# Optimization experiments

Hardware: AMD Instinct MI355X
Metric: run time of the kernel (lower is better)

## Reference

```python
import jax, jax.numpy as jnp
import numpy as np

NUM_HEADS = 8
NUM_POINTS = 4


def setup_inputs() -> dict:
    key = jax.random.key(0)
    bs, h, w = 2, 128, 128
    cin = cout = 256
    nq = h * w
    ks = jax.random.split(key, 6)
    query = jax.random.normal(ks[0], (bs, nq, cin), jnp.float32)
    value = jax.random.normal(ks[1], (bs, nq, cin), jnp.float32)
    # sampling_offsets: small random weight, bias = directional grid init (as in init_weights)
    W_off = jax.random.normal(ks[2], (cin, NUM_HEADS * NUM_POINTS * 2), jnp.float32) * 0.01
    thetas = np.arange(NUM_HEADS, dtype=np.float32) * (2.0 * np.pi / NUM_HEADS)
    grid = np.stack([np.cos(thetas), np.sin(thetas)], -1)
    grid = grid / np.abs(grid).max(-1, keepdims=True)
    grid = np.tile(grid[:, None, :], (1, NUM_POINTS, 1)) * (np.arange(NUM_POINTS, dtype=np.float32)[None, :, None] + 1.0)
    b_off = jnp.asarray(grid.reshape(-1), jnp.float32)
    W_attn = jax.random.normal(ks[3], (cin, NUM_HEADS * NUM_POINTS), jnp.float32) * 0.01
    b_attn = jnp.zeros((NUM_HEADS * NUM_POINTS,), jnp.float32)
    s = 1.0 / np.sqrt(cin)  # xavier-ish uniform
    W_val = jax.random.uniform(ks[4], (cin, cout), jnp.float32, -s, s)
    b_val = jnp.zeros((cout,), jnp.float32)
    W_out = jax.random.uniform(ks[5], (cout, cout), jnp.float32, -s, s)
    b_out = jnp.zeros((cout,), jnp.float32)
    return {"query": query, "value": value, "W_off": W_off, "b_off": b_off,
            "W_attn": W_attn, "b_attn": b_attn, "W_val": W_val, "b_val": b_val,
            "W_out": W_out, "b_out": b_out, "h": h, "w": w}


def _bilinear_sample(v_flat, ix, iy, h, w):
    # v_flat: (bs, heads, h*w, d); ix/iy: (bs, heads, nq, P) pixel coords.
    # grid_sample bilinear, align_corners=False, padding_mode='zeros'.
    x0 = jnp.floor(ix)
    y0 = jnp.floor(iy)
    wx1 = ix - x0
    wy1 = iy - y0
    bs, hd, nq, P = ix.shape
    acc = 0.0
    corners = ((x0, y0, (1.0 - wx1) * (1.0 - wy1)),
               (x0 + 1.0, y0, wx1 * (1.0 - wy1)),
               (x0, y0 + 1.0, (1.0 - wx1) * wy1),
               (x0 + 1.0, y0 + 1.0, wx1 * wy1))
    for xc, yc, wgt in corners:
        xi = xc.astype(jnp.int32)
        yi = yc.astype(jnp.int32)
        valid = (xi >= 0) & (xi < w) & (yi >= 0) & (yi < h)
        idx = jnp.clip(yi, 0, h - 1) * w + jnp.clip(xi, 0, w - 1)
        g = jnp.take_along_axis(v_flat, idx.reshape(bs, hd, nq * P)[..., None], axis=2)
        acc = acc + g.reshape(bs, hd, nq, P, -1) * (wgt * valid)[..., None]
    return acc  # (bs, heads, nq, P, d)


def deform_attn(query, value, W_off, b_off, W_attn, b_attn, W_val, b_val, h, w):
    bs, nq, _ = query.shape
    d = W_val.shape[1] // NUM_HEADS
    v = (value @ W_val + b_val).reshape(bs, nq, NUM_HEADS, d)
    off = (query @ W_off + b_off).reshape(bs, nq, NUM_HEADS, NUM_POINTS, 2)
    aw = jax.nn.softmax((query @ W_attn + b_attn).reshape(bs, nq, NUM_HEADS, NUM_POINTS), axis=-1)
    # reference points in [0,1], scale_ratio=1.0, (x, y) order
    ys = (jnp.arange(h, dtype=jnp.float32) + 0.5) / h
    xs = (jnp.arange(w, dtype=jnp.float32) + 0.5) / w
    ry, rx = jnp.meshgrid(ys, xs, indexing='ij')
    ref = jnp.stack([rx.reshape(-1), ry.reshape(-1)], -1)  # (nq, 2)
    loc = ref[None, :, None, None, :] + off / jnp.array([w, h], jnp.float32)
    grid = 2.0 * loc - 1.0  # normalized grid_sample coords
    grid = grid.transpose(0, 2, 1, 3, 4)  # (bs, heads, nq, P, 2)
    ix = (grid[..., 0] + 1.0) * (w / 2.0) - 0.5
    iy = (grid[..., 1] + 1.0) * (h / 2.0) - 0.5
    v_flat = v.transpose(0, 2, 1, 3)  # (bs, heads, h*w, d)
    sampled = _bilinear_sample(v_flat, ix, iy, h, w)  # (bs, heads, nq, P, d)
    out = (sampled * aw.transpose(0, 2, 1, 3)[..., None]).sum(3)  # (bs, heads, nq, d)
    return out.transpose(0, 2, 1, 3).reshape(bs, nq, NUM_HEADS * d)


def reference(query, value, W_off, b_off, W_attn, b_attn, W_val, b_val, W_out, b_out, h, w):
    attn = deform_attn(query, value, W_off, b_off, W_attn, b_attn, W_val, b_val, h, w)
    # dropout acts as identity in eval mode; identity residual = query
    return attn @ W_out + b_out + query
```

## Files before the change

kernel.cpp:

```cpp
#include <hip/hip_runtime.h>
#include <type_traits>

#define H_IMG 128
#define W_IMG 128
#define NQ (H_IMG * W_IMG)
#define CIN 256
#define NH 8
#define NP 4
#define DH 32
#define LDSP 264

typedef __bf16 bf16x4 __attribute__((ext_vector_type(4)));
typedef __bf16 bf16x8 __attribute__((ext_vector_type(8)));
typedef float f32x4 __attribute__((ext_vector_type(4)));

__global__ __launch_bounds__(256) void prep_weights(
    const float* __restrict__ Wval, const float* __restrict__ Wout,
    const float* __restrict__ Woff, const float* __restrict__ Wattn,
    const float* __restrict__ boff, const float* __restrict__ battn,
    __bf16* __restrict__ btv, __bf16* __restrict__ bto,
    __bf16* __restrict__ btoa, float* __restrict__ bias96) {
  int id = blockIdx.x * 256 + threadIdx.x;
  if (id < 256 * 256) {
    int n = id >> 8, k = id & 255;
    btv[n * 256 + k] = (__bf16)Wval[k * 256 + n];
    bto[n * 256 + k] = (__bf16)Wout[k * 256 + n];
  }
  if (id < 96 * 256) {
    int n = id >> 8, k = id & 255;
    float w = (n < 64) ? Woff[k * 64 + n] : Wattn[k * 32 + (n - 64)];
    btoa[n * 256 + k] = (__bf16)w;
  }
  if (id < 96) {
    bias96[id] = (id < 64) ? boff[id] : battn[id - 64];
  }
}

template <typename TA, typename TC, bool PLANAR, bool ADD>
__global__ __launch_bounds__(256) void gemm64(
    const TA* __restrict__ A, const __bf16* __restrict__ BT,
    const float* __restrict__ bias, const float* __restrict__ addm,
    TC* __restrict__ C, int M) {
  const int t = threadIdx.x;
  const int lane = t & 63;
  const int wave = t >> 6;
  const int r = lane & 15;
  const int q = lane >> 4;
  const int gm0 = blockIdx.x * 64;
  const int gn0 = blockIdx.y * 64;
  const int wm = (wave & 1) * 32;
  const int wn = (wave >> 1) * 32;

  __shared__ __bf16 As[64 * LDSP];
  __shared__ __bf16 Bs[64 * LDSP];

  if constexpr (std::is_same<TA, float>::value) {
#pragma unroll
    for (int i = 0; i < 16; ++i) {
      int g = i * 256 + t;
      int row = g >> 6, c4 = g & 63;
      float4 f = *(const float4*)(A + (size_t)(gm0 + row) * 256 + c4 * 4);
      bf16x4 hh;
      hh[0] = (__bf16)f.x; hh[1] = (__bf16)f.y;
      hh[2] = (__bf16)f.z; hh[3] = (__bf16)f.w;
      *(bf16x4*)(&As[row * LDSP + c4 * 4]) = hh;
    }
  } else {
#pragma unroll
    for (int i = 0; i < 8; ++i) {
      int g = i * 256 + t;
      int row = g >> 5, c = g & 31;
      *(bf16x8*)(&As[row * LDSP + c * 8]) =
          *(const bf16x8*)(A + (size_t)(gm0 + row) * 256 + c * 8);
    }
  }
#pragma unroll
  for (int i = 0; i < 8; ++i) {
    int g = i * 256 + t;
    int row = g >> 5, c = g & 31;
    *(bf16x8*)(&Bs[row * LDSP + c * 8]) =
        *(const bf16x8*)(BT + (size_t)(gn0 + row) * 256 + c * 8);
  }
  __syncthreads();

  f32x4 acc[2][2];
#pragma unroll
  for (int mt = 0; mt < 2; ++mt)
#pragma unroll
    for (int nt = 0; nt < 2; ++nt) acc[mt][nt] = (f32x4){0.f, 0.f, 0.f, 0.f};

#pragma unroll
  for (int kt = 0; kt < 8; ++kt) {
    const int ko = kt * 32 + q * 8;
    bf16x8 a0 = *(const bf16x8*)(&As[(wm + r) * LDSP + ko]);
    bf16x8 a1 = *(const bf16x8*)(&As[(wm + 16 + r) * LDSP + ko]);
    bf16x8 b0 = *(const bf16x8*)(&Bs[(wn + r) * LDSP + ko]);
    bf16x8 b1 = *(const bf16x8*)(&Bs[(wn + 16 + r) * LDSP + ko]);
    acc[0][0] = __builtin_amdgcn_mfma_f32_16x16x32_bf16(a0, b0, acc[0][0], 0, 0, 0);
    acc[0][1] = __builtin_amdgcn_mfma_f32_16x16x32_bf16(a0, b1, acc[0][1], 0, 0, 0);
    acc[1][0] = __builtin_amdgcn_mfma_f32_16x16x32_bf16(a1, b0, acc[1][0], 0, 0, 0);
    acc[1][1] = __builtin_amdgcn_mfma_f32_16x16x32_bf16(a1, b1, acc[1][1], 0, 0, 0);
  }

#pragma unroll
  for (int mt = 0; mt < 2; ++mt)
#pragma unroll
    for (int nt = 0; nt < 2; ++nt)
#pragma unroll
      for (int rr = 0; rr < 4; ++rr) {
        int row = gm0 + wm + mt * 16 + q * 4 + rr;
        int col = gn0 + wn + nt * 16 + r;
        float val = acc[mt][nt][rr] + bias[col];
        if constexpr (ADD) val += addm[(size_t)row * 256 + col];
        if constexpr (PLANAR)
          C[((size_t)(col >> 5) * M + row) * 32 + (col & 31)] = (TC)val;
        else
          C[(size_t)row * 256 + col] = (TC)val;
      }
}

__global__ __launch_bounds__(256) void oa_sample(
    const float* __restrict__ query, const __bf16* __restrict__ btoa,
    const float* __restrict__ bias96, const __bf16* __restrict__ v,
    __bf16* __restrict__ attn, int M) {
  const int t = threadIdx.x;
  const int lane = t & 63;
  const int wave = t >> 6;
  const int r = lane & 15;
  const int q = lane >> 4;
  const int gm0 = blockIdx.x * 64;
  const int wm = (wave & 1) * 32;
  const int n0 = (wave >> 1) * 48;

  __shared__ __bf16 As[64 * LDSP];
  __shared__ float oas[64 * 100];

#pragma unroll
  for (int i = 0; i < 16; ++i) {
    int g = i * 256 + t;
    int row = g >> 6, c4 = g & 63;
    float4 f = *(const float4*)(query + (size_t)(gm0 + row) * 256 + c4 * 4);
    bf16x4 hh;
    hh[0] = (__bf16)f.x; hh[1] = (__bf16)f.y;
    hh[2] = (__bf16)f.z; hh[3] = (__bf16)f.w;
    *(bf16x4*)(&As[row * LDSP + c4 * 4]) = hh;
  }
  __syncthreads();

  f32x4 acc[2][3];
#pragma unroll
  for (int mt = 0; mt < 2; ++mt)
#pragma unroll
    for (int nt = 0; nt < 3; ++nt) acc[mt][nt] = (f32x4){0.f, 0.f, 0.f, 0.f};

#pragma unroll
  for (int kt = 0; kt < 8; ++kt) {
    const int ko = kt * 32 + q * 8;
    bf16x8 a0 = *(const bf16x8*)(&As[(wm + r) * LDSP + ko]);
    bf16x8 a1 = *(const bf16x8*)(&As[(wm + 16 + r) * LDSP + ko]);
    bf16x8 b[3];
#pragma unroll
    for (int nt = 0; nt < 3; ++nt)
      b[nt] = *(const bf16x8*)(btoa + (size_t)(n0 + nt * 16 + r) * 256 + ko);
#pragma unroll
    for (int nt = 0; nt < 3; ++nt) {
      acc[0][nt] = __builtin_amdgcn_mfma_f32_16x16x32_bf16(a0, b[nt], acc[0][nt], 0, 0, 0);
      acc[1][nt] = __builtin_amdgcn_mfma_f32_16x16x32_bf16(a1, b[nt], acc[1][nt], 0, 0, 0);
    }
  }
#pragma unroll
  for (int mt = 0; mt < 2; ++mt)
#pragma unroll
    for (int nt = 0; nt < 3; ++nt)
#pragma unroll
      for (int rr = 0; rr < 4; ++rr) {
        int rl = wm + mt * 16 + q * 4 + rr;
        int col = n0 + nt * 16 + r;
        oas[rl * 100 + col] = acc[mt][nt][rr] + bias96[col];
      }
  __syncthreads();

  const int qrow = t >> 2;
  const int c8 = (t & 3) * 8;
  const int row = gm0 + qrow;
  const int b = row >> 14;
  const int qi = row & (NQ - 1);
  const int x = qi & (W_IMG - 1);
  const int y = qi >> 7;
  const float* oar = &oas[qrow * 100];
#pragma unroll
  for (int h = 0; h < NH; ++h) {
    float l0 = oar[64 + h * 4 + 0];
    float l1 = oar[64 + h * 4 + 1];
    float l2 = oar[64 + h * 4 + 2];
    float l3 = oar[64 + h * 4 + 3];
    float mx = fmaxf(fmaxf(l0, l1), fmaxf(l2, l3));
    float e0 = __expf(l0 - mx), e1 = __expf(l1 - mx);
    float e2 = __expf(l2 - mx), e3 = __expf(l3 - mx);
    float inv = 1.f / (e0 + e1 + e2 + e3);
    float awp[4] = {e0 * inv, e1 * inv, e2 * inv, e3 * inv};
    float fa[8] = {0.f, 0.f, 0.f, 0.f, 0.f, 0.f, 0.f, 0.f};
    const __bf16* vh = v + ((size_t)h * M + (size_t)b * NQ) * 32 + c8;
#pragma unroll
    for (int p = 0; p < NP; ++p) {
      float ox = oar[h * 8 + p * 2 + 0];
      float oy = oar[h * 8 + p * 2 + 1];
      float ix = (float)x + ox;
      float iy = (float)y + oy;
      float x0f = floorf(ix), y0f = floorf(iy);
      float wx1 = ix - x0f, wy1 = iy - y0f;
      int x0 = (int)x0f, y0 = (int)y0f;
      float wgt[4] = {(1.f - wx1) * (1.f - wy1), wx1 * (1.f - wy1),
                      (1.f - wx1) * wy1, wx1 * wy1};
      int xs[4] = {x0, x0 + 1, x0, x0 + 1};
      int ysv[4] = {y0, y0, y0 + 1, y0 + 1};
#pragma unroll
      for (int c = 0; c < 4; ++c) {
        int xi = xs[c], yi = ysv[c];
        bool valid = (xi >= 0) & (xi < W_IMG) & (yi >= 0) & (yi < H_IMG);
        int xc = xi < 0 ? 0 : (xi > W_IMG - 1 ? W_IMG - 1 : xi);
        int yc = yi < 0 ? 0 : (yi > H_IMG - 1 ? H_IMG - 1 : yi);
        float wv = awp[p] * wgt[c] * (valid ? 1.f : 0.f);
        bf16x8 g = *(const bf16x8*)(vh + (size_t)(yc * W_IMG + xc) * 32);
#pragma unroll
        for (int j = 0; j < 8; ++j) fa[j] += wv * (float)g[j];
      }
    }
    bf16x8 o;
#pragma unroll
    for (int j = 0; j < 8; ++j) o[j] = (__bf16)fa[j];
    *(bf16x8*)(attn + (size_t)row * 256 + h * DH + c8) = o;
  }
}

extern "C" void kernel_launch(void* const* d_in, const int* in_sizes, int n_in,
                              void* d_out, int out_size, void* d_ws, size_t ws_size,
                              hipStream_t stream) {
  const float* query  = (const float*)d_in[0];
  const float* value  = (const float*)d_in[1];
  const float* W_off  = (const float*)d_in[2];
  const float* b_off  = (const float*)d_in[3];
  const float* W_attn = (const float*)d_in[4];
  const float* b_attn = (const float*)d_in[5];
  const float* W_val  = (const float*)d_in[6];
  const float* b_val  = (const float*)d_in[7];
  const float* W_out  = (const float*)d_in[8];
  const float* b_out  = (const float*)d_in[9];
  float* out = (float*)d_out;

  char* ws = (char*)d_ws;
  __bf16* btv    = (__bf16*)(ws + 0);
  __bf16* bto    = (__bf16*)(ws + 131072);
  __bf16* btoa   = (__bf16*)(ws + 262144);
  float*  bias96 = (float*)(ws + 311296);
  __bf16* v      = (__bf16*)(ws + 524288);
  __bf16* attn   = (__bf16*)(ws + 17301504);

  const int M = in_sizes[0] / CIN;

  prep_weights<<<256, 256, 0, stream>>>(W_val, W_out, W_off, W_attn,
                                        b_off, b_attn, btv, bto, btoa, bias96);
  gemm64<float, __bf16, true, false><<<dim3(M / 64, 4), 256, 0, stream>>>(
      value, btv, b_val, nullptr, v, M);
  oa_sample<<<M / 64, 256, 0, stream>>>(query, btoa, bias96, v, attn, M);
  gemm64<__bf16, float, false, true><<<dim3(M / 64, 4), 256, 0, stream>>>(
      attn, bto, b_out, query, out, M);
}
```

Before: 175.0 us.

## Fuse output projection into sampling kernel and widen value GEMM tiles

```diff
diff --git a/kernel.cpp b/kernel.cpp
--- a/kernel.cpp
+++ b/kernel.cpp
@@ -1,5 +1,4 @@
 #include <hip/hip_runtime.h>
-#include <type_traits>
 
 #define H_IMG 128
 #define W_IMG 128
@@ -36,101 +35,79 @@
   }
 }
 
-template <typename TA, typename TC, bool PLANAR, bool ADD>
-__global__ __launch_bounds__(256) void gemm64(
-    const TA* __restrict__ A, const __bf16* __restrict__ BT,
-    const float* __restrict__ bias, const float* __restrict__ addm,
-    TC* __restrict__ C, int M) {
+__global__ __launch_bounds__(256) void gemm_v(
+    const float* __restrict__ A, const __bf16* __restrict__ BT,
+    const float* __restrict__ bias, __bf16* __restrict__ v, int M) {
   const int t = threadIdx.x;
   const int lane = t & 63;
   const int wave = t >> 6;
   const int r = lane & 15;
   const int q = lane >> 4;
   const int gm0 = blockIdx.x * 64;
-  const int gn0 = blockIdx.y * 64;
-  const int wm = (wave & 1) * 32;
-  const int wn = (wave >> 1) * 32;
+  const int wn = wave * 64;
 
   __shared__ __bf16 As[64 * LDSP];
-  __shared__ __bf16 Bs[64 * LDSP];
-
-  if constexpr (std::is_same<TA, float>::value) {
-#pragma unroll
-    for (int i = 0; i < 16; ++i) {
-      int g = i * 256 + t;
-      int row = g >> 6, c4 = g & 63;
-      float4 f = *(const float4*)(A + (size_t)(gm0 + row) * 256 + c4 * 4);
-      bf16x4 hh;
-      hh[0] = (__bf16)f.x; hh[1] = (__bf16)f.y;
-      hh[2] = (__bf16)f.z; hh[3] = (__bf16)f.w;
-      *(bf16x4*)(&As[row * LDSP + c4 * 4]) = hh;
-    }
-  } else {
-#pragma unroll
-    for (int i = 0; i < 8; ++i) {
-      int g = i * 256 + t;
-      int row = g >> 5, c = g & 31;
-      *(bf16x8*)(&As[row * LDSP + c * 8]) =
-          *(const bf16x8*)(A + (size_t)(gm0 + row) * 256 + c * 8);
-    }
-  }
-#pragma unroll
-  for (int i = 0; i < 8; ++i) {
+
+#pragma unroll
+  for (int i = 0; i < 16; ++i) {
     int g = i * 256 + t;
-    int row = g >> 5, c = g & 31;
-    *(bf16x8*)(&Bs[row * LDSP + c * 8]) =
-        *(const bf16x8*)(BT + (size_t)(gn0 + row) * 256 + c * 8);
-  }
-  __syncthreads();
-
-  f32x4 acc[2][2];
-#pragma unroll
-  for (int mt = 0; mt < 2; ++mt)
-#pragma unroll
-    for (int nt = 0; nt < 2; ++nt) acc[mt][nt] = (f32x4){0.f, 0.f, 0.f, 0.f};
+    int row = g >> 6, c4 = g & 63;
+    float4 f = *(const float4*)(A + (size_t)(gm0 + row) * 256 + c4 * 4);
+    bf16x4 hh;
+    hh[0] = (__bf16)f.x; hh[1] = (__bf16)f.y;
+    hh[2] = (__bf16)f.z; hh[3] = (__bf16)f.w;
+    *(bf16x4*)(&As[row * LDSP + c4 * 4]) = hh;
+  }
+  __syncthreads();
+
+  f32x4 acc[4][4];
+#pragma unroll
+  for (int mt = 0; mt < 4; ++mt)
+#pragma unroll
+    for (int nt = 0; nt < 4; ++nt) acc[mt][nt] = (f32x4){0.f, 0.f, 0.f, 0.f};
 
 #pragma unroll
   for (int kt = 0; kt < 8; ++kt) {
     const int ko = kt * 32 + q * 8;
-    bf16x8 a0 = *(const bf16x8*)(&As[(wm + r) * LDSP + ko]);
-    bf16x8 a1 = *(const bf16x8*)(&As[(wm + 16 + r) * LDSP + ko]);
-    bf16x8 b0 = *(const bf16x8*)(&Bs[(wn + r) * LDSP + ko]);
-    bf16x8 b1 = *(const bf16x8*)(&Bs[(wn + 16 + r) * LDSP + ko]);
-    acc[0][0] = __builtin_amdgcn_mfma_f32_16x16x32_bf16(a0, b0, acc[0][0], 0, 0, 0);
-    acc[0][1] = __builtin_amdgcn_mfma_f32_16x16x32_bf16(a0, b1, acc[0][1], 0, 0, 0);
-    acc[1][0] = __builtin_amdgcn_mfma_f32_16x16x32_bf16(a1, b0, acc[1][0], 0, 0, 0);
-    acc[1][1] = __builtin_amdgcn_mfma_f32_16x16x32_bf16(a1, b1, acc[1][1], 0, 0, 0);
-  }
-
-#pragma unroll
-  for (int mt = 0; mt < 2; ++mt)
-#pragma unroll
-    for (int nt = 0; nt < 2; ++nt)
+    bf16x8 a[4], b[4];
+#pragma unroll
+    for (int mt = 0; mt < 4; ++mt)
+      a[mt] = *(const bf16x8*)(&As[(mt * 16 + r) * LDSP + ko]);
+#pragma unroll
+    for (int nt = 0; nt < 4; ++nt)
+      b[nt] = *(const bf16x8*)(BT + (size_t)(wn + nt * 16 + r) * 256 + ko);
+#pragma unroll
+    for (int mt = 0; mt < 4; ++mt)
+#pragma unroll
+      for (int nt = 0; nt < 4; ++nt)
+        acc[mt][nt] =
+            __builtin_amdgcn_mfma_f32_16x16x32_bf16(a[mt], b[nt], acc[mt][nt], 0, 0, 0);
+  }
+
+#pragma unroll
+  for (int mt = 0; mt < 4; ++mt)
+#pragma unroll
+    for (int nt = 0; nt < 4; ++nt)
 #pragma unroll
       for (int rr = 0; rr < 4; ++rr) {
-        int row = gm0 + wm + mt * 16 + q * 4 + rr;
-        int col = gn0 + wn + nt * 16 + r;
-        float val = acc[mt][nt][rr] + bias[col];
-        if constexpr (ADD) val += addm[(size_t)row * 256 + col];
-        if constexpr (PLANAR)
-          C[((size_t)(col >> 5) * M + row) * 32 + (col & 31)] = (TC)val;
-        else
-          C[(size_t)row * 256 + col] = (TC)val;
+        int row = gm0 + mt * 16 + q * 4 + rr;
+        int col = wn + nt * 16 + r;
+        v[((size_t)(col >> 5) * M + row) * 32 + (col & 31)] =
+            (__bf16)(acc[mt][nt][rr] + bias[col]);
       }
 }
 
-__global__ __launch_bounds__(256) void oa_sample(
+__global__ __launch_bounds__(256) void oa_sample_out(
     const float* __restrict__ query, const __bf16* __restrict__ btoa,
     const float* __restrict__ bias96, const __bf16* __restrict__ v,
-    __bf16* __restrict__ attn, int M) {
+    const __bf16* __restrict__ bto, const float* __restrict__ b_out,
+    float* __restrict__ out, int M) {
   const int t = threadIdx.x;
   const int lane = t & 63;
   const int wave = t >> 6;
   const int r = lane & 15;
   const int q = lane >> 4;
   const int gm0 = blockIdx.x * 64;
-  const int wm = (wave & 1) * 32;
-  const int n0 = (wave >> 1) * 48;
 
   __shared__ __bf16 As[64 * LDSP];
   __shared__ float oas[64 * 100];
@@ -147,89 +124,132 @@
   }
   __syncthreads();
 
-  f32x4 acc[2][3];
-#pragma unroll
-  for (int mt = 0; mt < 2; ++mt)
-#pragma unroll
-    for (int nt = 0; nt < 3; ++nt) acc[mt][nt] = (f32x4){0.f, 0.f, 0.f, 0.f};
-
-#pragma unroll
-  for (int kt = 0; kt < 8; ++kt) {
-    const int ko = kt * 32 + q * 8;
-    bf16x8 a0 = *(const bf16x8*)(&As[(wm + r) * LDSP + ko]);
-    bf16x8 a1 = *(const bf16x8*)(&As[(wm + 16 + r) * LDSP + ko]);
-    bf16x8 b[3];
-#pragma unroll
-    for (int nt = 0; nt < 3; ++nt)
-      b[nt] = *(const bf16x8*)(btoa + (size_t)(n0 + nt * 16 + r) * 256 + ko);
-#pragma unroll
-    for (int nt = 0; nt < 3; ++nt) {
-      acc[0][nt] = __builtin_amdgcn_mfma_f32_16x16x32_bf16(a0, b[nt], acc[0][nt], 0, 0, 0);
-      acc[1][nt] = __builtin_amdgcn_mfma_f32_16x16x32_bf16(a1, b[nt], acc[1][nt], 0, 0, 0);
-    }
-  }
-#pragma unroll
-  for (int mt = 0; mt < 2; ++mt)
-#pragma unroll
-    for (int nt = 0; nt < 3; ++nt)
-#pragma unroll
-      for (int rr = 0; rr < 4; ++rr) {
-        int rl = wm + mt * 16 + q * 4 + rr;
-        int col = n0 + nt * 16 + r;
-        oas[rl * 100 + col] = acc[mt][nt][rr] + bias96[col];
-      }
-  __syncthreads();
-
-  const int qrow = t >> 2;
-  const int c8 = (t & 3) * 8;
-  const int row = gm0 + qrow;
-  const int b = row >> 14;
-  const int qi = row & (NQ - 1);
-  const int x = qi & (W_IMG - 1);
-  const int y = qi >> 7;
-  const float* oar = &oas[qrow * 100];
-#pragma unroll
-  for (int h = 0; h < NH; ++h) {
-    float l0 = oar[64 + h * 4 + 0];
-    float l1 = oar[64 + h * 4 + 1];
-    float l2 = oar[64 + h * 4 + 2];
-    float l3 = oar[64 + h * 4 + 3];
-    float mx = fmaxf(fmaxf(l0, l1), fmaxf(l2, l3));
-    float e0 = __expf(l0 - mx), e1 = __expf(l1 - mx);
-    float e2 = __expf(l2 - mx), e3 = __expf(l3 - mx);
-    float inv = 1.f / (e0 + e1 + e2 + e3);
-    float awp[4] = {e0 * inv, e1 * inv, e2 * inv, e3 * inv};
-    float fa[8] = {0.f, 0.f, 0.f, 0.f, 0.f, 0.f, 0.f, 0.f};
-    const __bf16* vh = v + ((size_t)h * M + (size_t)b * NQ) * 32 + c8;
-#pragma unroll
-    for (int p = 0; p < NP; ++p) {
-      float ox = oar[h * 8 + p * 2 + 0];
-      float oy = oar[h * 8 + p * 2 + 1];
-      float ix = (float)x + ox;
-      float iy = (float)y + oy;
-      float x0f = floorf(ix), y0f = floorf(iy);
-      float wx1 = ix - x0f, wy1 = iy - y0f;
-      int x0 = (int)x0f, y0 = (int)y0f;
-      float wgt[4] = {(1.f - wx1) * (1.f - wy1), wx1 * (1.f - wy1),
-                      (1.f - wx1) * wy1, wx1 * wy1};
-      int xs[4] = {x0, x0 + 1, x0, x0 + 1};
-      int ysv[4] = {y0, y0, y0 + 1, y0 + 1};
-#pragma unroll
-      for (int c = 0; c < 4; ++c) {
-        int xi = xs[c], yi = ysv[c];
-        bool valid = (xi >= 0) & (xi < W_IMG) & (yi >= 0) & (yi < H_IMG);
-        int xc = xi < 0 ? 0 : (xi > W_IMG - 1 ? W_IMG - 1 : xi);
-        int yc = yi < 0 ? 0 : (yi > H_IMG - 1 ? H_IMG - 1 : yi);
-        float wv = awp[p] * wgt[c] * (valid ? 1.f : 0.f);
-        bf16x8 g = *(const bf16x8*)(vh + (size_t)(yc * W_IMG + xc) * 32);
-#pragma unroll
-        for (int j = 0; j < 8; ++j) fa[j] += wv * (float)g[j];
+  {
+    const int wm = (wave & 1) * 32;
+    const int n0 = (wave >> 1) * 48;
+    f32x4 acc[2][3];
+#pragma unroll
+    for (int mt = 0; mt < 2; ++mt)
+#pragma unroll
+      for (int nt = 0; nt < 3; ++nt) acc[mt][nt] = (f32x4){0.f, 0.f, 0.f, 0.f};
+#pragma unroll
+    for (int kt = 0; kt < 8; ++kt) {
+      const int ko = kt * 32 + q * 8;
+      bf16x8 a0 = *(const bf16x8*)(&As[(wm + r) * LDSP + ko]);
+      bf16x8 a1 = *(const bf16x8*)(&As[(wm + 16 + r) * LDSP + ko]);
+      bf16x8 b[3];
+#pragma unroll
+      for (int nt = 0; nt < 3; ++nt)
+        b[nt] = *(const bf16x8*)(btoa + (size_t)(n0 + nt * 16 + r) * 256 + ko);
+#pragma unroll
+      for (int nt = 0; nt < 3; ++nt) {
+        acc[0][nt] = __builtin_amdgcn_mfma_f32_16x16x32_bf16(a0, b[nt], acc[0][nt], 0, 0, 0);
+        acc[1][nt] = __builtin_amdgcn_mfma_f32_16x16x32_bf16(a1, b[nt], acc[1][nt], 0, 0, 0);
       }
     }
-    bf16x8 o;
-#pragma unroll
-    for (int j = 0; j < 8; ++j) o[j] = (__bf16)fa[j];
-    *(bf16x8*)(attn + (size_t)row * 256 + h * DH + c8) = o;
+#pragma unroll
+    for (int mt = 0; mt < 2; ++mt)
+#pragma unroll
+      for (int nt = 0; nt < 3; ++nt)
+#pragma unroll
+        for (int rr = 0; rr < 4; ++rr) {
+          int rl = wm + mt * 16 + q * 4 + rr;
+          int col = n0 + nt * 16 + r;
+          oas[rl * 100 + col] = acc[mt][nt][rr] + bias96[col];
+        }
+  }
+  __syncthreads();
+
+  {
+    const int qrow = t >> 2;
+    const int c8 = (t & 3) * 8;
+    const int row = gm0 + qrow;
+    const int b = row >> 14;
+    const int qi = row & (NQ - 1);
+    const int x = qi & (W_IMG - 1);
+    const int y = qi >> 7;
+    const float* oar = &oas[qrow * 100];
+#pragma unroll
+    for (int h = 0; h < NH; ++h) {
+      float l0 = oar[64 + h * 4 + 0];
+      float l1 = oar[64 + h * 4 + 1];
+      float l2 = oar[64 + h * 4 + 2];
+      float l3 = oar[64 + h * 4 + 3];
+      float mx = fmaxf(fmaxf(l0, l1), fmaxf(l2, l3));
+      float e0 = __expf(l0 - mx), e1 = __expf(l1 - mx);
+      float e2 = __expf(l2 - mx), e3 = __expf(l3 - mx);
+      float inv = 1.f / (e0 + e1 + e2 + e3);
+      float awp[4] = {e0 * inv, e1 * inv, e2 * inv, e3 * inv};
+      float fa[8] = {0.f, 0.f, 0.f, 0.f, 0.f, 0.f, 0.f, 0.f};
+      const __bf16* vh = v + ((size_t)h * M + (size_t)b * NQ) * 32 + c8;
+#pragma unroll
+      for (int p = 0; p < NP; ++p) {
+        float ox = oar[h * 8 + p * 2 + 0];
+        float oy = oar[h * 8 + p * 2 + 1];
+        float ix = (float)x + ox;
+        float iy = (float)y + oy;
+        float x0f = floorf(ix), y0f = floorf(iy);
+        float wx1 = ix - x0f, wy1 = iy - y0f;
+        int x0 = (int)x0f, y0 = (int)y0f;
+        float wgt[4] = {(1.f - wx1) * (1.f - wy1), wx1 * (1.f - wy1),
+                        (1.f - wx1) * wy1, wx1 * wy1};
+        int xs[4] = {x0, x0 + 1, x0, x0 + 1};
+        int ysv[4] = {y0, y0, y0 + 1, y0 + 1};
+#pragma unroll
+        for (int c = 0; c < 4; ++c) {
+          int xi = xs[c], yi = ysv[c];
+          bool valid = (xi >= 0) & (xi < W_IMG) & (yi >= 0) & (yi < H_IMG);
+          int xc = xi < 0 ? 0 : (xi > W_IMG - 1 ? W_IMG - 1 : xi);
+          int yc = yi < 0 ? 0 : (yi > H_IMG - 1 ? H_IMG - 1 : yi);
+          float wv = awp[p] * wgt[c] * (valid ? 1.f : 0.f);
+          bf16x8 g = *(const bf16x8*)(vh + (size_t)(yc * W_IMG + xc) * 32);
+#pragma unroll
+          for (int j = 0; j < 8; ++j) fa[j] += wv * (float)g[j];
+        }
+      }
+      bf16x8 o;
+#pragma unroll
+      for (int j = 0; j < 8; ++j) o[j] = (__bf16)fa[j];
+      *(bf16x8*)(&As[qrow * LDSP + h * DH + c8]) = o;
+    }
+  }
+  __syncthreads();
+
+  {
+    const int wn = wave * 64;
+    f32x4 acc[4][4];
+#pragma unroll
+    for (int mt = 0; mt < 4; ++mt)
+#pragma unroll
+      for (int nt = 0; nt < 4; ++nt) acc[mt][nt] = (f32x4){0.f, 0.f, 0.f, 0.f};
+#pragma unroll
+    for (int kt = 0; kt < 8; ++kt) {
+      const int ko = kt * 32 + q * 8;
+      bf16x8 a[4], b[4];
+#pragma unroll
+      for (int mt = 0; mt < 4; ++mt)
+        a[mt] = *(const bf16x8*)(&As[(mt * 16 + r) * LDSP + ko]);
+#pragma unroll
+      for (int nt = 0; nt < 4; ++nt)
+        b[nt] = *(const bf16x8*)(bto + (size_t)(wn + nt * 16 + r) * 256 + ko);
+#pragma unroll
+      for (int mt = 0; mt < 4; ++mt)
+#pragma unroll
+        for (int nt = 0; nt < 4; ++nt)
+          acc[mt][nt] =
+              __builtin_amdgcn_mfma_f32_16x16x32_bf16(a[mt], b[nt], acc[mt][nt], 0, 0, 0);
+    }
+#pragma unroll
+    for (int mt = 0; mt < 4; ++mt)
+#pragma unroll
+      for (int nt = 0; nt < 4; ++nt)
+#pragma unroll
+        for (int rr = 0; rr < 4; ++rr) {
+          int row = gm0 + mt * 16 + q * 4 + rr;
+          int col = wn + nt * 16 + r;
+          out[(size_t)row * 256 + col] =
+              acc[mt][nt][rr] + b_out[col] + query[(size_t)row * 256 + col];
+        }
   }
 }
 
@@ -254,15 +274,11 @@
   __bf16* btoa   = (__bf16*)(ws + 262144);
   float*  bias96 = (float*)(ws + 311296);
   __bf16* v      = (__bf16*)(ws + 524288);
-  __bf16* attn   = (__bf16*)(ws + 17301504);
 
   const int M = in_sizes[0] / CIN;
 
   prep_weights<<<256, 256, 0, stream>>>(W_val, W_out, W_off, W_attn,
                                         b_off, b_attn, btv, bto, btoa, bias96);
-  gemm64<float, __bf16, true, false><<<dim3(M / 64, 4), 256, 0, stream>>>(
-      value, btv, b_val, nullptr, v, M);
-  oa_sample<<<M / 64, 256, 0, stream>>>(query, btoa, bias96, v, attn, M);
-  gemm64<__bf16, float, false, true><<<dim3(M / 64, 4), 256, 0, stream>>>(
-      attn, bto, b_out, query, out, M);
-}
+  gemm_v<<<M / 64, 256, 0, stream>>>(value, btv, b_val, v, M);
+  oa_sample_out<<<M / 64, 256, 0, stream>>>(query, btoa, bias96, v, bto, b_out, out, M);
+}
```

Measured after the change: 167.6 us. -4.2%, faster.
